# Kernel optimization log

Hardware: AMD Instinct MI355X
Metric: run time of the kernel (lower is better)

Reference implementation:

```python
import jax, jax.numpy as jnp
from jax import lax
import numpy as np

B, T, E, H, DA, HEADS, V = 128, 512, 256, 256, 25, 5, 2080
NEG = -1e30


def setup_inputs() -> dict:
    key = jax.random.key(0)
    ks = jax.random.split(key, 10)
    word_ids = jax.random.randint(ks[0], (B, T), 0, V)
    lengths = jax.random.randint(ks[1], (B,), 1, T + 1)  # >=1, original skips empty captions
    emb = jax.random.normal(ks[2], (V, E), dtype=jnp.float32)  # normal_(0,1) init
    sc = 0.05
    W_ih_f = jax.random.normal(ks[3], (4 * H, E), dtype=jnp.float32) * sc
    W_hh_f = jax.random.normal(ks[4], (4 * H, H), dtype=jnp.float32) * sc
    W_ih_b = jax.random.normal(ks[5], (4 * H, E), dtype=jnp.float32) * sc
    W_hh_b = jax.random.normal(ks[6], (4 * H, H), dtype=jnp.float32) * sc
    b_f = jnp.zeros((4 * H,), jnp.float32)  # biases init constant 0
    b_b = jnp.zeros((4 * H,), jnp.float32)
    W_s1 = jax.random.normal(ks[7], (DA, 2 * H), dtype=jnp.float32) * sc
    W_s2 = jax.random.normal(ks[8], (HEADS, DA), dtype=jnp.float32) * sc
    return dict(word_ids=word_ids, lengths=lengths, emb=emb,
                W_ih_f=W_ih_f, W_hh_f=W_hh_f, b_f=b_f,
                W_ih_b=W_ih_b, W_hh_b=W_hh_b, b_b=b_b,
                W_s1=W_s1, W_s2=W_s2)


def _lstm(x, W_ih, W_hh, b):
    # x: [B,T,E] -> outputs [B,T,H]; PyTorch gate order i,f,g,o; zero init state
    px = jnp.einsum('bte,ge->tbg', x, W_ih) + b  # [T,B,4H], input proj precomputed
    h0 = jnp.zeros((x.shape[0], W_hh.shape[1]), x.dtype)

    def step(carry, p):
        h, c = carry
        g = p + h @ W_hh.T
        i, f, gg, o = jnp.split(g, 4, axis=-1)
        c = jax.nn.sigmoid(f) * c + jax.nn.sigmoid(i) * jnp.tanh(gg)
        h = jax.nn.sigmoid(o) * jnp.tanh(c)
        return (h, c), h

    _, hs = lax.scan(step, (h0, h0), px)
    return hs.transpose(1, 0, 2)  # [B,T,H]


def _forward(word_ids, lengths, emb, W_ih_f, W_hh_f, b_f, W_ih_b, W_hh_b, b_b, W_s1, W_s2):
    x = emb[word_ids]  # [B,T,E]
    tpos = jnp.arange(T)
    mask = tpos[None, :] < lengths[:, None]  # [B,T] valid positions
    # per-sample reversal within its own length (garbage tail comes after valid prefix)
    rev_idx = jnp.clip(lengths[:, None] - 1 - tpos[None, :], 0)  # [B,T]
    x_rev = jnp.take_along_axis(x, rev_idx[:, :, None], axis=1)
    h_fwd = _lstm(x, W_ih_f, W_hh_f, b_f)                       # [B,T,H]
    h_bwd_rev = _lstm(x_rev, W_ih_b, W_hh_b, b_b)
    h_bwd = jnp.take_along_axis(h_bwd_rev, rev_idx[:, :, None], axis=1)  # back to original order
    Hc = jnp.concatenate([h_fwd, h_bwd], axis=-1)               # [B,T,2H]
    # attention: softmax over time per head, masked to valid length
    s = jnp.tanh(Hc @ W_s1.T) @ W_s2.T                          # [B,T,heads]
    logits = jnp.where(mask[:, :, None], s, NEG)
    A = jax.nn.softmax(logits, axis=1).transpose(0, 2, 1)       # [B,heads,T]
    A = A * mask[:, None, :].astype(A.dtype)                    # exact zeros outside length
    M = jnp.einsum('bht,btd->bhd', A, Hc)                       # [B,heads,2H]
    sentence_embeddings = M.reshape(M.shape[0], -1)             # [B, heads*2H]
    AAt = jnp.einsum('bht,bgt->bhg', A, A)
    AAt = AAt * (1.0 - jnp.eye(HEADS, dtype=AAt.dtype))         # zero diagonal
    penal = jnp.sum(AAt * AAt) / M.shape[0]                     # mean of Frobenius^2
    return sentence_embeddings, penal


def reference(word_ids, lengths, emb, W_ih_f, W_hh_f, b_f, W_ih_b, W_hh_b, b_b, W_s1, W_s2):
    return _forward(word_ids, lengths, emb, W_ih_f, W_hh_f, b_f, W_ih_b, W_hh_b, b_b, W_s1, W_s2)
```

## Files before the change

kernel.cpp:

```cpp
#include <hip/hip_runtime.h>
#include <math.h>

#define T 512
#define B 128
#define E 256
#define H 256
#define G 1024
#define DA 25
#define HEADS 5
#define V 2080
#define NEGINF (-1e30f)

static constexpr size_t WBT_OFF  = 0;
static constexpr size_t WIH_OFF  = 1048576;
static constexpr size_t WS1M_OFF = 2097152;
static constexpr size_t PX_OFF   = 2148352;
static constexpr size_t HC_OFF   = 69257216;
static constexpr size_t HBUF_OFF = 203474944;
static constexpr size_t CST_OFF  = 203737088;
static constexpr size_t A_OFF    = 203999232;
static constexpr size_t PART_OFF = 205309952;
static constexpr size_t EMBH_OFF = 205310464;
static constexpr size_t EMBH_END = EMBH_OFF + (size_t)V * E * 2;

static constexpr unsigned LSTM_LDS_BYTES = 160304;

typedef _Float16 half2v __attribute__((ext_vector_type(2)));
typedef _Float16 half8_ __attribute__((ext_vector_type(8)));
typedef float    f32x4  __attribute__((ext_vector_type(4)));

#if __has_builtin(__builtin_amdgcn_exp2f)
#define EXP2F_(x) __builtin_amdgcn_exp2f(x)
#else
#define EXP2F_(x) exp2f(x)
#endif
#if __has_builtin(__builtin_amdgcn_rcpf)
#define RCPF_(x) __builtin_amdgcn_rcpf(x)
#else
#define RCPF_(x) (1.0f / (x))
#endif

__device__ __forceinline__ float sigmoidf_(float x) { return 1.f / (1.f + expf(-x)); }

__device__ __forceinline__ float sigmoid_fast_(float x) {
    return RCPF_(1.f + EXP2F_(-1.44269504f * x));
}
__device__ __forceinline__ float tanh_fast_(float x) {
    return 1.f - 2.f * RCPF_(1.f + EXP2F_(2.88539008f * x));
}

__device__ __forceinline__ unsigned short f2h_(float f) {
    _Float16 h = (_Float16)f;
    unsigned short u;
    __builtin_memcpy(&u, &h, 2);
    return u;
}

__device__ __forceinline__ float fdot2_(unsigned w, half2v h, float acc) {
#if __has_builtin(__builtin_amdgcn_fdot2)
    half2v wv;
    __builtin_memcpy(&wv, &w, 4);
    return __builtin_amdgcn_fdot2(wv, h, acc, false);
#else
    unsigned short lo = (unsigned short)(w & 0xffffu), hi = (unsigned short)(w >> 16);
    _Float16 w0, w1;
    __builtin_memcpy(&w0, &lo, 2);
    __builtin_memcpy(&w1, &hi, 2);
    return fmaf((float)w0, (float)h[0], fmaf((float)w1, (float)h[1], acc));
#endif
}

__device__ __forceinline__ half2v packh2_(float a, float b) {
    half2v h;
    h[0] = (_Float16)a;
    h[1] = (_Float16)b;
    return h;
}

__global__ __launch_bounds__(256) void prep_kernel(const float* __restrict__ Whf,
                                                   const float* __restrict__ Whb,
                                                   const float* __restrict__ Wif,
                                                   const float* __restrict__ Wib,
                                                   const float* __restrict__ Ws1,
                                                   const float* __restrict__ emb,
                                                   unsigned short* __restrict__ wbt,
                                                   unsigned short* __restrict__ wih,
                                                   unsigned short* __restrict__ ws1m,
                                                   unsigned short* __restrict__ embh) {
    int idx = blockIdx.x * 256 + threadIdx.x;
    if (idx < 2 * G * H) {
        int d = idx >> 18;
        int rem = idx & 262143;
        int r = rem >> 8;
        int k = rem & 255;
        const float* W = d ? Whb : Whf;
        int gate = r >> 8, j = r & 255;
        int k2 = k >> 1, ke = k & 1;
        wbt[(((size_t)d * 128 + k2) * 256 + j) * 8 + gate * 2 + ke] = f2h_(W[(size_t)r * H + k]);
        const float* Wi = d ? Wib : Wif;
        wih[((size_t)d * G + r) * 256 + k] = f2h_(Wi[(size_t)r * E + k]);
    }
    if (idx < 32 * 512) {
        int r = idx >> 9, k = idx & 511;
        ws1m[idx] = (r < DA) ? f2h_(Ws1[r * 512 + k]) : (unsigned short)0;
    }
    if (embh && idx < V * E) embh[idx] = f2h_(emb[idx]);
}

__global__ __launch_bounds__(256) void proj_kernel(const int* __restrict__ word_ids,
                                                   const int* __restrict__ lengths,
                                                   const float* __restrict__ emb,
                                                   const unsigned* __restrict__ embh,
                                                   const unsigned* __restrict__ wih,
                                                   const float* __restrict__ bf,
                                                   const float* __restrict__ bb,
                                                   float* __restrict__ pxc, int chunk) {
    int g0 = blockIdx.x * 64;
    int b  = blockIdx.y;
    int d  = blockIdx.z;
    int len = lengths[b];
    int t0 = chunk * 64;
    if (t0 >= len) return;
    const float* bias = d ? bb : bf;

    __shared__ _Float16 A_s[64][264];
    __shared__ _Float16 B_s[64][264];

    int tid = threadIdx.x;
    int sr = tid >> 2, sq = tid & 3;

    {
        int t = t0 + sr;
        int src = d ? max(len - 1 - t, 0) : t;
        int wid = word_ids[b * T + src];
        if (embh) {
            const uint4* ap = (const uint4*)embh + (size_t)wid * 32;
            #pragma unroll
            for (int c = 0; c < 8; c++) {
                uint4 v = ap[sq * 8 + c];
                *(uint4*)&A_s[sr][(sq * 8 + c) * 8] = v;
            }
        } else {
            const float4* ep = (const float4*)(emb + (size_t)wid * E);
            #pragma unroll
            for (int c = 0; c < 8; c++) {
                float4 x0 = ep[(sq * 8 + c) * 2];
                float4 x1 = ep[(sq * 8 + c) * 2 + 1];
                half8_ hv;
                hv[0] = (_Float16)x0.x; hv[1] = (_Float16)x0.y;
                hv[2] = (_Float16)x0.z; hv[3] = (_Float16)x0.w;
                hv[4] = (_Float16)x1.x; hv[5] = (_Float16)x1.y;
                hv[6] = (_Float16)x1.z; hv[7] = (_Float16)x1.w;
                *(half8_*)&A_s[sr][(sq * 8 + c) * 8] = hv;
            }
        }
        const uint4* bp = (const uint4*)wih + ((size_t)d * G + g0 + sr) * 32;
        #pragma unroll
        for (int c = 0; c < 8; c++) {
            uint4 v = bp[sq * 8 + c];
            *(uint4*)&B_s[sr][(sq * 8 + c) * 8] = v;
        }
    }
    __syncthreads();

    int lane = tid & 63, wave = tid >> 6;
    int m0 = (wave >> 1) * 32;
    int n0 = (wave & 1) * 32;
    int lr = lane & 15, lq = lane >> 4;

    f32x4 acc00 = {0.f, 0.f, 0.f, 0.f}, acc01 = {0.f, 0.f, 0.f, 0.f};
    f32x4 acc10 = {0.f, 0.f, 0.f, 0.f}, acc11 = {0.f, 0.f, 0.f, 0.f};

    #pragma unroll
    for (int k0 = 0; k0 < E; k0 += 32) {
        int ka = k0 + lq * 8;
        half8_ af0 = *(const half8_*)&A_s[m0 + lr][ka];
        half8_ af1 = *(const half8_*)&A_s[m0 + 16 + lr][ka];
        half8_ bf0 = *(const half8_*)&B_s[n0 + lr][ka];
        half8_ bf1 = *(const half8_*)&B_s[n0 + 16 + lr][ka];
        acc00 = __builtin_amdgcn_mfma_f32_16x16x32_f16(af0, bf0, acc00, 0, 0, 0);
        acc01 = __builtin_amdgcn_mfma_f32_16x16x32_f16(af0, bf1, acc01, 0, 0, 0);
        acc10 = __builtin_amdgcn_mfma_f32_16x16x32_f16(af1, bf0, acc10, 0, 0, 0);
        acc11 = __builtin_amdgcn_mfma_f32_16x16x32_f16(af1, bf1, acc11, 0, 0, 0);
    }

    float bia0 = bias[g0 + n0 + lr];
    float bia1 = bias[g0 + n0 + 16 + lr];
    #pragma unroll
    for (int mi = 0; mi < 2; mi++) {
        f32x4 ar0 = mi ? acc10 : acc00;
        f32x4 ar1 = mi ? acc11 : acc01;
        #pragma unroll
        for (int rr = 0; rr < 4; rr++) {
            int s = m0 + mi * 16 + lq * 4 + rr;
            float* dst = pxc + ((size_t)(d * 64 + s) * B + b) * G + g0;
            dst[n0 + lr]      = ar0[rr] + bia0;
            dst[n0 + 16 + lr] = ar1[rr] + bia1;
        }
    }
}

__global__ __launch_bounds__(1024, 4) void lstm6_kernel(const int* __restrict__ lengths,
                                                        const unsigned* __restrict__ wbt,
                                                        const float* __restrict__ pxc,
                                                        float* __restrict__ hc_out,
                                                        float* __restrict__ hbuf,
                                                        float* __restrict__ cstate,
                                                        int chunk) {
    int b   = blockIdx.x;
    int d   = blockIdx.y;
    int tid = threadIdx.x;
    int j  = tid & 255;
    int kq = tid >> 8;

    int len = lengths[b];
    int t0 = chunk * 64;
    if (t0 >= len) return;
    int tend = min(t0 + 64, len);

    extern __shared__ char smem[];
    unsigned* hh   = (unsigned*)smem;
    float4*   part = (float4*)(smem + 512);
    uint4*    wst  = (uint4*)(smem + 12848);
    unsigned short* hh16 = (unsigned short*)smem;

    float* hbufg = hbuf + ((size_t)d * B + b) * 256;

    float c = 0.f, hreg = 0.f;
    if (chunk == 0) {
        if (tid < 128) hh[tid] = 0u;
    } else {
        if (kq == 0) c = cstate[((size_t)d * B + b) * H + j];
        if (tid < 128) {
            half2v hv2 = packh2_(hbufg[2 * tid], hbufg[2 * tid + 1]);
            unsigned hu;
            __builtin_memcpy(&hu, &hv2, 4);
            hh[tid] = hu;
        }
    }

    const uint4* wp  = (const uint4*)wbt + ((size_t)d * 128 + kq * 32) * 256 + j;
    const float* pxd = pxc + (size_t)d * 64 * B * G;

    #pragma unroll
    for (int r = 0; r < 9; r++)
        wst[(kq * 9 + r) * 256 + j] = wp[(size_t)r * 256];
    uint4 wr0  = wp[9 * 256],  wr1  = wp[10 * 256], wr2  = wp[11 * 256];
    uint4 wr3  = wp[12 * 256], wr4  = wp[13 * 256], wr5  = wp[14 * 256];
    uint4 wr6  = wp[15 * 256], wr7  = wp[16 * 256], wr8  = wp[17 * 256];
    uint4 wr9  = wp[18 * 256], wr10 = wp[19 * 256], wr11 = wp[20 * 256];
    uint4 wr12 = wp[21 * 256], wr13 = wp[22 * 256], wr14 = wp[23 * 256];
    __syncthreads();

    int hlane = kq * 32 + (tid & 31);
    int pendpos = -1;

    for (int t = t0; t < tend; t++) {
        int s = t - t0;

        if (kq == 0 && pendpos >= 0)
            hc_out[((size_t)b * T + pendpos) * (2 * H) + d * H + j] = hreg;

        float p0, p1, p2, p3;
        if (kq == 0) {
            const float* pxs = pxd + ((size_t)s * B + b) * G;
            p0 = pxs[j];
            p1 = pxs[256 + j];
            p2 = pxs[512 + j];
            p3 = pxs[768 + j];
        }

        unsigned hlv = hh[hlane];
        uint4 wv0 = wp[24 * 256], wv1 = wp[25 * 256], wv2 = wp[26 * 256], wv3 = wp[27 * 256];

        float a0 = 0.f, a1 = 0.f, a2 = 0.f, a3 = 0.f;

        #define HROW(IDX) __builtin_amdgcn_readlane(hlv, IDX)
        #define DOT4(WV, IDX)                                          \
            { unsigned hu = HROW(IDX); half2v hx;                      \
              __builtin_memcpy(&hx, &hu, 4);                           \
              a0 = fdot2_(WV.x, hx, a0); a1 = fdot2_(WV.y, hx, a1);    \
              a2 = fdot2_(WV.z, hx, a2); a3 = fdot2_(WV.w, hx, a3); }

        #pragma unroll
        for (int r = 0; r < 9; r++) {
            uint4 wv = wst[(kq * 9 + r) * 256 + j];
            DOT4(wv, r)
        }
        DOT4(wv0, 24) DOT4(wv1, 25) DOT4(wv2, 26) DOT4(wv3, 27)
        uint4 wv4 = wp[28 * 256], wv5 = wp[29 * 256], wv6 = wp[30 * 256], wv7 = wp[31 * 256];
        DOT4(wr0, 9)  DOT4(wr1, 10)  DOT4(wr2, 11)  DOT4(wr3, 12)
        DOT4(wr4, 13) DOT4(wr5, 14)  DOT4(wr6, 15)  DOT4(wr7, 16)
        DOT4(wr8, 17) DOT4(wr9, 18)  DOT4(wr10, 19) DOT4(wr11, 20)
        DOT4(wr12, 21) DOT4(wr13, 22) DOT4(wr14, 23)
        DOT4(wv4, 28) DOT4(wv5, 29) DOT4(wv6, 30) DOT4(wv7, 31)
        #undef DOT4
        #undef HROW

        if (kq > 0) part[(kq - 1) * 257 + j] = make_float4(a0, a1, a2, a3);
        __syncthreads();

        if (kq == 0) {
            __builtin_amdgcn_s_setprio(1);
            #pragma unroll
            for (int q = 0; q < 3; q++) {
                float4 qv = part[q * 257 + j];
                a0 += qv.x; a1 += qv.y; a2 += qv.z; a3 += qv.w;
            }
            a0 += p0; a1 += p1; a2 += p2; a3 += p3;

            float ig = sigmoid_fast_(a0), fg = sigmoid_fast_(a1), og = sigmoid_fast_(a3);
            c = fg * c + ig * tanh_fast_(a2);
            float h = og * tanh_fast_(c);
            hreg = h;
            hh16[j] = f2h_(h);
            pendpos = d ? (len - 1 - t) : t;
            __builtin_amdgcn_s_setprio(0);
        }
        __syncthreads();
    }

    if (kq == 0) {
        if (pendpos >= 0)
            hc_out[((size_t)b * T + pendpos) * (2 * H) + d * H + j] = hreg;
        cstate[((size_t)d * B + b) * H + j] = c;
        hbufg[j] = hreg;
    }
}

__global__ __launch_bounds__(256) void logits_kernel(const int* __restrict__ lengths,
                                                     const float* __restrict__ hc,
                                                     const uint4* __restrict__ ws1m,
                                                     const float* __restrict__ Ws2,
                                                     float* __restrict__ S) {
    __shared__ _Float16 A_s[64][520];
    __shared__ _Float16 B_s[32][520];

    int b = blockIdx.y, tt = blockIdx.x;
    int tid = threadIdx.x;
    int len = lengths[b];
    int t0 = tt * 64;

    int lane = tid & 63, wave = tid >> 6;
    int lr = lane & 15, lq = lane >> 4;
    int m0 = wave * 16;

    if (t0 >= len) {
        if (lr < HEADS) {
            #pragma unroll
            for (int rr = 0; rr < 4; rr++) {
                int t = t0 + m0 + lq * 4 + rr;
                S[((size_t)b * HEADS + lr) * T + t] = NEGINF;
            }
        }
        return;
    }

    {
        #pragma unroll
        for (int i = 0; i < 8; i++) {
            int u = tid + i * 256;
            int r = u >> 6, c8 = u & 63;
            *(uint4*)&B_s[r][c8 * 8] = ws1m[u];
        }
    }
    {
        int row = tid >> 2, q = tid & 3;
        int t = t0 + row;
        const float4* ep = (const float4*)(hc + ((size_t)b * T + t) * 512 + q * 128);
        #pragma unroll
        for (int c = 0; c < 16; c++) {
            float4 x0 = ep[2 * c];
            float4 x1 = ep[2 * c + 1];
            half8_ hv;
            hv[0] = (_Float16)x0.x; hv[1] = (_Float16)x0.y;
            hv[2] = (_Float16)x0.z; hv[3] = (_Float16)x0.w;
            hv[4] = (_Float16)x1.x; hv[5] = (_Float16)x1.y;
            hv[6] = (_Float16)x1.z; hv[7] = (_Float16)x1.w;
            *(half8_*)&A_s[row][q * 128 + c * 8] = hv;
        }
    }
    __syncthreads();

    f32x4 acc0 = {0.f, 0.f, 0.f, 0.f};
    f32x4 acc1 = {0.f, 0.f, 0.f, 0.f};
    #pragma unroll
    for (int ks = 0; ks < 16; ks++) {
        int ka = ks * 32 + lq * 8;
        half8_ af  = *(const half8_*)&A_s[m0 + lr][ka];
        half8_ bf0 = *(const half8_*)&B_s[lr][ka];
        half8_ bf1 = *(const half8_*)&B_s[16 + lr][ka];
        acc0 = __builtin_amdgcn_mfma_f32_16x16x32_f16(af, bf0, acc0, 0, 0, 0);
        acc1 = __builtin_amdgcn_mfma_f32_16x16x32_f16(af, bf1, acc1, 0, 0, 0);
    }

    float w2a[HEADS], w2b[HEADS];
    #pragma unroll
    for (int h = 0; h < HEADS; h++) {
        w2a[h] = Ws2[h * DA + lr];
        w2b[h] = (lr + 16 < DA) ? Ws2[h * DA + 16 + lr] : 0.f;
    }

    #pragma unroll
    for (int rr = 0; rr < 4; rr++) {
        float y0 = tanhf(acc0[rr]);
        float y1 = tanhf(acc1[rr]);
        int t = t0 + m0 + lq * 4 + rr;
        float sv[HEADS];
        #pragma unroll
        for (int h = 0; h < HEADS; h++) {
            float v = y0 * w2a[h] + y1 * w2b[h];
            v += __shfl_xor(v, 1, 16);
            v += __shfl_xor(v, 2, 16);
            v += __shfl_xor(v, 4, 16);
            v += __shfl_xor(v, 8, 16);
            sv[h] = v;
        }
        if (lr < HEADS) {
            S[((size_t)b * HEADS + lr) * T + t] = (t < len) ? sv[lr] : NEGINF;
        }
    }
}

__global__ __launch_bounds__(256) void softmax_kernel(float* __restrict__ S) {
    int row = blockIdx.x;
    float* p = S + (size_t)row * T;
    int tid = threadIdx.x;
    int lane = tid & 63, wave = tid >> 6;
    __shared__ float rr[4], ss[4];

    float mx = NEGINF;
    #pragma unroll
    for (int i = 0; i < 2; i++) mx = fmaxf(mx, p[tid + i * 256]);
    for (int off = 32; off; off >>= 1) mx = fmaxf(mx, __shfl_xor(mx, off, 64));
    if (lane == 0) rr[wave] = mx;
    __syncthreads();
    mx = fmaxf(fmaxf(rr[0], rr[1]), fmaxf(rr[2], rr[3]));

    float e[2], sum = 0.f;
    #pragma unroll
    for (int i = 0; i < 2; i++) { e[i] = expf(p[tid + i * 256] - mx); sum += e[i]; }
    for (int off = 32; off; off >>= 1) sum += __shfl_xor(sum, off, 64);
    if (lane == 0) ss[wave] = sum;
    __syncthreads();
    sum = ss[0] + ss[1] + ss[2] + ss[3];
    float inv = 1.f / sum;
    #pragma unroll
    for (int i = 0; i < 2; i++) p[tid + i * 256] = e[i] * inv;
}

__global__ __launch_bounds__(256) void attnM_kernel(const int* __restrict__ lengths,
                                                    const float* __restrict__ A,
                                                    const float* __restrict__ hc,
                                                    float* __restrict__ out,
                                                    float* __restrict__ part) {
    int b = blockIdx.x, tid = threadIdx.x;
    int len = lengths[b];
    const float* Ab  = A + (size_t)b * HEADS * T;
    const float* hcb = hc + (size_t)b * T * (2 * H);
    float acc[HEADS][2];
    #pragma unroll
    for (int h = 0; h < HEADS; h++) { acc[h][0] = 0.f; acc[h][1] = 0.f; }
    float p[10];
    #pragma unroll
    for (int i = 0; i < 10; i++) p[i] = 0.f;

    for (int t = 0; t < len; t++) {
        float v0 = hcb[(size_t)t * (2 * H) + tid];
        float v1 = hcb[(size_t)t * (2 * H) + H + tid];
        float a0 = Ab[t], a1 = Ab[T + t], a2 = Ab[2 * T + t], a3 = Ab[3 * T + t], a4 = Ab[4 * T + t];
        acc[0][0] += a0 * v0; acc[0][1] += a0 * v1;
        acc[1][0] += a1 * v0; acc[1][1] += a1 * v1;
        acc[2][0] += a2 * v0; acc[2][1] += a2 * v1;
        acc[3][0] += a3 * v0; acc[3][1] += a3 * v1;
        acc[4][0] += a4 * v0; acc[4][1] += a4 * v1;
        if ((t & 255) == tid) {
            p[0] += a0 * a1; p[1] += a0 * a2; p[2] += a0 * a3; p[3] += a0 * a4;
            p[4] += a1 * a2; p[5] += a1 * a3; p[6] += a1 * a4;
            p[7] += a2 * a3; p[8] += a2 * a4; p[9] += a3 * a4;
        }
    }
    #pragma unroll
    for (int h = 0; h < HEADS; h++) {
        out[(size_t)b * (HEADS * 2 * H) + h * (2 * H) + tid]     = acc[h][0];
        out[(size_t)b * (HEADS * 2 * H) + h * (2 * H) + H + tid] = acc[h][1];
    }

    __shared__ float red[10][4];
    int lane = tid & 63, wave = tid >> 6;
    #pragma unroll
    for (int i = 0; i < 10; i++) {
        float v = p[i];
        for (int off = 32; off; off >>= 1) v += __shfl_xor(v, off, 64);
        if (lane == 0) red[i][wave] = v;
    }
    __syncthreads();
    if (tid == 0) {
        float s = 0.f;
        #pragma unroll
        for (int i = 0; i < 10; i++) {
            float P = red[i][0] + red[i][1] + red[i][2] + red[i][3];
            s += 2.f * P * P;
        }
        part[b] = s;
    }
}

__global__ __launch_bounds__(128) void final_kernel(const float* __restrict__ part,
                                                    float* __restrict__ out) {
    int tid = threadIdx.x;
    float v = part[tid];
    for (int off = 32; off; off >>= 1) v += __shfl_xor(v, off, 64);
    __shared__ float r2[2];
    if ((tid & 63) == 0) r2[tid >> 6] = v;
    __syncthreads();
    if (tid == 0) out[(size_t)B * HEADS * 2 * H] = (r2[0] + r2[1]) * (1.f / (float)B);
}

extern "C" void kernel_launch(void* const* d_in, const int* in_sizes, int n_in,
                              void* d_out, int out_size, void* d_ws, size_t ws_size,
                              hipStream_t stream) {
    const int*   word_ids = (const int*)d_in[0];
    const int*   lengths  = (const int*)d_in[1];
    const float* emb      = (const float*)d_in[2];
    const float* W_ih_f   = (const float*)d_in[3];
    const float* W_hh_f   = (const float*)d_in[4];
    const float* b_f      = (const float*)d_in[5];
    const float* W_ih_b   = (const float*)d_in[6];
    const float* W_hh_b   = (const float*)d_in[7];
    const float* b_b      = (const float*)d_in[8];
    const float* W_s1     = (const float*)d_in[9];
    const float* W_s2     = (const float*)d_in[10];
    float* out = (float*)d_out;

    char* ws = (char*)d_ws;
    unsigned short* wbt16 = (unsigned short*)(ws + WBT_OFF);
    unsigned*       wbt   = (unsigned*)(ws + WBT_OFF);
    unsigned short* wih16 = (unsigned short*)(ws + WIH_OFF);
    unsigned*       wihu  = (unsigned*)(ws + WIH_OFF);
    unsigned short* ws1m16 = (unsigned short*)(ws + WS1M_OFF);
    const uint4*    ws1m4  = (const uint4*)(ws + WS1M_OFF);
    float* pxc    = (float*)(ws + PX_OFF);
    float* hc     = (float*)(ws + HC_OFF);
    float* hbuf   = (float*)(ws + HBUF_OFF);
    float* cstate = (float*)(ws + CST_OFF);
    float* Abuf   = (float*)(ws + A_OFF);
    float* part   = (float*)(ws + PART_OFF);
    bool have_embh = (ws_size >= EMBH_END);
    unsigned short* embh16 = have_embh ? (unsigned short*)(ws + EMBH_OFF) : nullptr;
    const unsigned* embhu  = have_embh ? (const unsigned*)(ws + EMBH_OFF) : nullptr;

    prep_kernel<<<2080, 256, 0, stream>>>(W_hh_f, W_hh_b, W_ih_f, W_ih_b, W_s1, emb,
                                          wbt16, wih16, ws1m16, embh16);

    for (int c = 0; c < 8; c++) {
        proj_kernel<<<dim3(16, 128, 2), 256, 0, stream>>>(
            word_ids, lengths, emb, embhu, wihu, b_f, b_b, pxc, c);
        lstm6_kernel<<<dim3(128, 2), 1024, LSTM_LDS_BYTES, stream>>>(
            lengths, wbt, pxc, hc, hbuf, cstate, c);
    }

    logits_kernel<<<dim3(8, 128), 256, 0, stream>>>(lengths, hc, ws1m4, W_s2, Abuf);
    softmax_kernel<<<B * HEADS, 256, 0, stream>>>(Abuf);
    attnM_kernel<<<B, 256, 0, stream>>>(lengths, Abuf, hc, out, part);
    final_kernel<<<1, 128, 0, stream>>>(part, out);
}
```

Baseline: 1.303 ms.

## Split attention-weighted sum over time chunks with a separate reduction kernel

The attention pooling kernel previously ran one block per batch sample and looped serially over up to 512 timesteps. It now launches 8 time-chunk blocks per sample, each writing partial head sums and partial A·Aᵀ products to workspace (reusing the px buffer). A new reduce kernel sums the chunks and finishes the penalty term. This exposes 8x more parallelism for a small stage, at the cost of one extra launch and some partial-buffer traffic.

```diff
diff --git a/kernel.cpp b/kernel.cpp
--- a/kernel.cpp
+++ b/kernel.cpp
@@ -22,6 +22,8 @@
 static constexpr size_t PART_OFF = 205309952;
 static constexpr size_t EMBH_OFF = 205310464;
 static constexpr size_t EMBH_END = EMBH_OFF + (size_t)V * E * 2;
+static constexpr size_t PM_OFF   = PX_OFF;
+static constexpr size_t PP_OFF   = PX_OFF + 10485760;
 
 static constexpr unsigned LSTM_LDS_BYTES = 160304;
 
@@ -449,13 +451,15 @@
     for (int i = 0; i < 2; i++) p[tid + i * 256] = e[i] * inv;
 }
 
-__global__ __launch_bounds__(256) void attnM_kernel(const int* __restrict__ lengths,
-                                                    const float* __restrict__ A,
-                                                    const float* __restrict__ hc,
-                                                    float* __restrict__ out,
-                                                    float* __restrict__ part) {
-    int b = blockIdx.x, tid = threadIdx.x;
+__global__ __launch_bounds__(256) void attnM_part_kernel(const int* __restrict__ lengths,
+                                                         const float* __restrict__ A,
+                                                         const float* __restrict__ hc,
+                                                         float* __restrict__ pm,
+                                                         float* __restrict__ pp) {
+    int tc = blockIdx.x, b = blockIdx.y, tid = threadIdx.x;
     int len = lengths[b];
+    int t0 = tc * 64;
+    int tend = min(t0 + 64, len);
     const float* Ab  = A + (size_t)b * HEADS * T;
     const float* hcb = hc + (size_t)b * T * (2 * H);
     float acc[HEADS][2];
@@ -465,7 +469,7 @@
     #pragma unroll
     for (int i = 0; i < 10; i++) p[i] = 0.f;
 
-    for (int t = 0; t < len; t++) {
+    for (int t = t0; t < tend; t++) {
         float v0 = hcb[(size_t)t * (2 * H) + tid];
         float v1 = hcb[(size_t)t * (2 * H) + H + tid];
         float a0 = Ab[t], a1 = Ab[T + t], a2 = Ab[2 * T + t], a3 = Ab[3 * T + t], a4 = Ab[4 * T + t];
@@ -480,10 +484,11 @@
             p[7] += a2 * a3; p[8] += a2 * a4; p[9] += a3 * a4;
         }
     }
+    size_t base = ((size_t)tc * B + b) * (HEADS * 2 * H);
     #pragma unroll
     for (int h = 0; h < HEADS; h++) {
-        out[(size_t)b * (HEADS * 2 * H) + h * (2 * H) + tid]     = acc[h][0];
-        out[(size_t)b * (HEADS * 2 * H) + h * (2 * H) + H + tid] = acc[h][1];
+        pm[base + h * (2 * H) + tid]     = acc[h][0];
+        pm[base + h * (2 * H) + H + tid] = acc[h][1];
     }
 
     __shared__ float red[10][4];
@@ -495,13 +500,40 @@
         if (lane == 0) red[i][wave] = v;
     }
     __syncthreads();
+    if (tid < 10)
+        pp[((size_t)tc * B + b) * 16 + tid] =
+            red[tid][0] + red[tid][1] + red[tid][2] + red[tid][3];
+}
+
+__global__ __launch_bounds__(256) void attnM_reduce_kernel(const float* __restrict__ pm,
+                                                           const float* __restrict__ pp,
+                                                           float* __restrict__ out,
+                                                           float* __restrict__ part) {
+    int b = blockIdx.x, tid = threadIdx.x;
+    #pragma unroll
+    for (int h = 0; h < HEADS; h++) {
+        float a0 = 0.f, a1 = 0.f;
+        #pragma unroll
+        for (int tc = 0; tc < 8; tc++) {
+            size_t base = ((size_t)tc * B + b) * (HEADS * 2 * H) + h * (2 * H);
+            a0 += pm[base + tid];
+            a1 += pm[base + H + tid];
+        }
+        out[(size_t)b * (HEADS * 2 * H) + h * (2 * H) + tid]     = a0;
+        out[(size_t)b * (HEADS * 2 * H) + h * (2 * H) + H + tid] = a1;
+    }
+    __shared__ float sred[10];
+    if (tid < 10) {
+        float P = 0.f;
+        #pragma unroll
+        for (int tc = 0; tc < 8; tc++) P += pp[((size_t)tc * B + b) * 16 + tid];
+        sred[tid] = 2.f * P * P;
+    }
+    __syncthreads();
     if (tid == 0) {
         float s = 0.f;
         #pragma unroll
-        for (int i = 0; i < 10; i++) {
-            float P = red[i][0] + red[i][1] + red[i][2] + red[i][3];
-            s += 2.f * P * P;
-        }
+        for (int i = 0; i < 10; i++) s += sred[i];
         part[b] = s;
     }
 }
@@ -546,6 +578,8 @@
     float* cstate = (float*)(ws + CST_OFF);
     float* Abuf   = (float*)(ws + A_OFF);
     float* part   = (float*)(ws + PART_OFF);
+    float* pm     = (float*)(ws + PM_OFF);
+    float* pp     = (float*)(ws + PP_OFF);
     bool have_embh = (ws_size >= EMBH_END);
     unsigned short* embh16 = have_embh ? (unsigned short*)(ws + EMBH_OFF) : nullptr;
     const unsigned* embhu  = have_embh ? (const unsigned*)(ws + EMBH_OFF) : nullptr;
@@ -562,6 +596,7 @@
 
     logits_kernel<<<dim3(8, 128), 256, 0, stream>>>(lengths, hc, ws1m4, W_s2, Abuf);
     softmax_kernel<<<B * HEADS, 256, 0, stream>>>(Abuf);
-    attnM_kernel<<<B, 256, 0, stream>>>(lengths, Abuf, hc, out, part);
+    attnM_part_kernel<<<dim3(8, 128), 256, 0, stream>>>(lengths, Abuf, hc, pm, pp);
+    attnM_reduce_kernel<<<B, 256, 0, stream>>>(pm, pp, out, part);
     final_kernel<<<1, 128, 0, stream>>>(part, out);
 }
```

New measurement: 1.209 ms. 7.2% less time.
